# Performance work log

Hardware: AMD Instinct MI355X
Metric: run time of the kernel (lower is better)

The kernel has to match this reference:

```python
import jax, jax.numpy as jnp
import numpy as np


def setup_inputs() -> dict:
    key = jax.random.key(0)
    k1, k2, k3, k4 = jax.random.split(key, 4)
    B, T, N, C_IN, C_OUT, K = 32, 24, 1024, 64, 64, 3
    x = jax.random.normal(k1, (B, T, N, C_IN), dtype=jnp.float32)
    Tks = jax.random.normal(k2, (K, N, N), dtype=jnp.float32)
    # kaiming-uniform-ish init scale for Theta, small uniform bias
    bound_t = float(np.sqrt(6.0 / C_IN))
    Theta = jax.random.uniform(k3, (K, C_IN, C_OUT), dtype=jnp.float32,
                               minval=-bound_t, maxval=bound_t)
    bound_b = 1.0 / float(np.sqrt(C_IN))
    bias = jax.random.uniform(k4, (K, C_OUT), dtype=jnp.float32,
                              minval=-bound_b, maxval=bound_b)
    return {"x": x, "Tks": Tks, "Theta": Theta, "bias": bias}


def reference(x, Tks, Theta, bias):
    # torch.einsum('nn,btnc->btnc', T_k, x) extracts diag(T_k) and scales x per node.
    d = jnp.diagonal(Tks, axis1=1, axis2=2)  # [K, N]
    # sum_k diag(T_k) * x @ Theta_k  -> [B, T, N, C_OUT]
    out = jnp.einsum('kn,btnc,kco->btno', d, x, Theta)
    # each bias[k] is added once -> total additive term is sum over k
    out = out + jnp.sum(bias, axis=0)
    return out
```

## Files before the change

### kernel.cpp

```cpp
#include <hip/hip_runtime.h>


#define NNODES 1024
#define TILE_ROWS 64
#define NT 8
#define ROWS_PER_BLOCK (TILE_ROWS * NT)
#define NBLOCKS (786432 / ROWS_PER_BLOCK)

#define WS_W  0
#define WS_BS (24 * 1024)
#define WS_DV (24 * 1024 + 256)

typedef __attribute__((ext_vector_type(8))) short short8;
typedef __attribute__((ext_vector_type(4))) float f32x4;
typedef __attribute__((ext_vector_type(4))) int   i32x4;

__device__ __forceinline__ unsigned short f2bf(float f) {
    union { float f; unsigned u; } v; v.f = f;
    unsigned r = v.u + 0x7FFFu + ((v.u >> 16) & 1u);
    return (unsigned short)(r >> 16);
}

__device__ __forceinline__ int cvt_pk_bf16(float lo, float hi) {
    int r;
    asm("v_cvt_pk_bf16_f32 %0, %1, %2" : "=v"(r) : "v"(lo), "v"(hi));
    return r;
}

__device__ __forceinline__ void gload_lds16(const void* g, void* l) {
    __builtin_amdgcn_global_load_lds(
        (const __attribute__((address_space(1))) void*)g,
        (__attribute__((address_space(3))) void*)l,
        16, 0, 0);
}

__global__ void cheb_prep(const float* __restrict__ Tks,
                          const float* __restrict__ Theta,
                          const float* __restrict__ bias,
                          unsigned char* __restrict__ ws) {
    const int b = blockIdx.x;
    const int l = threadIdx.x;
    if (b < 24) {
        const int kc = b >> 3, h = (b >> 2) & 1, nb = b & 3;
        const int o  = nb * 16 + (l & 15);
        const int cb = h * 32 + (l >> 4) * 8;
        unsigned short* dst = (unsigned short*)(ws + WS_W) + ((size_t)b * 64 + l) * 8;
        #pragma unroll
        for (int j = 0; j < 8; ++j)
            dst[j] = f2bf(Theta[kc * 4096 + (cb + j) * 64 + o]);
    } else if (b < 40) {
        const int n = (b - 24) * 64 + l;
        const size_t dg = (size_t)n * (NNODES + 1);
        f32x4 v;
        v[0] = Tks[dg];
        v[1] = Tks[(size_t)NNODES * NNODES + dg];
        v[2] = Tks[(size_t)2 * NNODES * NNODES + dg];
        v[3] = 0.0f;
        *((f32x4*)(ws + WS_DV) + n) = v;
    } else {
        float* bs = (float*)(ws + WS_BS);
        bs[l] = bias[l] + bias[64 + l] + bias[128 + l];
    }
}

__global__ __launch_bounds__(512, 4) void cheb_main(
    const float* __restrict__ x,
    const unsigned char* __restrict__ ws,
    float* __restrict__ out)
{
    __shared__ float xs[4][TILE_ROWS * 64];
    __shared__ __align__(16) float dvs[ROWS_PER_BLOCK][4];

    const int tid  = threadIdx.x;
    const int wave = tid >> 6;
    const int lane = tid & 63;
    const int lrow = lane & 15;
    const int lgrp = lane >> 4;
    const int wr   = wave >> 1;
    const int q    = wave & 1;
    const size_t rowbase = (size_t)blockIdx.x * ROWS_PER_BLOCK;

    const unsigned short* wimg = (const unsigned short*)(ws + WS_W);
    const float*          bsum = (const float*)(ws + WS_BS);
    const f32x4*          dvec = (const f32x4*)(ws + WS_DV);

    short8 wf[3][2][2];
    #pragma unroll
    for (int kc = 0; kc < 3; ++kc)
        #pragma unroll
        for (int h = 0; h < 2; ++h)
            #pragma unroll
            for (int nb = 0; nb < 2; ++nb)
                wf[kc][h][nb] = *(const short8*)(
                    wimg + ((size_t)(((kc * 2 + h) * 4 + q * 2 + nb) * 64 + lane)) * 8);

    f32x4 bs4[2];
    #pragma unroll
    for (int nb = 0; nb < 2; ++nb)
        bs4[nb] = *(const f32x4*)(bsum + q * 32 + nb * 16 + lgrp * 4);

    gload_lds16((const char*)dvec + (((rowbase + wave * 64) & (NNODES - 1)) * 16 + lane * 16),
                &dvs[wave * 64][0]);

#define STAGE(T) do { if ((T) < NT) {                                         \
        _Pragma("unroll")                                                     \
        for (int s = 0; s < 2; ++s) {                                         \
            const int u_ = wave * 2 + s;                                      \
            const int R_ = u_ * 4 + lgrp;                                     \
            const int c_ = (lrow * 16) ^ ((R_ & 7) << 4);                     \
            const char* g_ = (const char*)x +                                 \
                (((rowbase + (size_t)(T) * TILE_ROWS + R_) << 8) + c_);       \
            gload_lds16(g_, (char*)&xs[(T) & 3][0] + u_ * 1024);              \
        } } } while (0)

#define WAITV(N) do {                                                         \
        asm volatile("s_waitcnt vmcnt(" #N ")" ::: "memory");                 \
        __builtin_amdgcn_sched_barrier(0);                                    \
        __builtin_amdgcn_s_barrier();                                         \
        __builtin_amdgcn_sched_barrier(0);                                    \
    } while (0)

#define BODY(T) do {                                                          \
        const int m_ = (lrow & 7) << 4;                                       \
        const char* rowp = (const char*)&xs[(T) & 3][0]                       \
                         + (wr * 16 + lrow) * 256;                            \
        const int c00 = (lgrp * 32) ^ m_;                                     \
        const int c01 = (lgrp * 32 + 16) ^ m_;                                \
        const f32x4 x0 = *(const f32x4*)(rowp + c00);                         \
        const f32x4 x1 = *(const f32x4*)(rowp + c01);                         \
        const f32x4 x2 = *(const f32x4*)(rowp + 128 + c00);                   \
        const f32x4 x3 = *(const f32x4*)(rowp + 128 + c01);                   \
        const f32x4 dv = *(const f32x4*)(&dvs[(T) * TILE_ROWS                 \
                                              + wr * 16 + lrow][0]);          \
        short8 xf[3][2];                                                      \
        _Pragma("unroll")                                                     \
        for (int kc = 0; kc < 3; ++kc) {                                      \
            const float dk = dv[kc];                                          \
            i32x4 r0, r1;                                                     \
            r0[0] = cvt_pk_bf16(dk * x0[0], dk * x0[1]);                      \
            r0[1] = cvt_pk_bf16(dk * x0[2], dk * x0[3]);                      \
            r0[2] = cvt_pk_bf16(dk * x1[0], dk * x1[1]);                      \
            r0[3] = cvt_pk_bf16(dk * x1[2], dk * x1[3]);                      \
            r1[0] = cvt_pk_bf16(dk * x2[0], dk * x2[1]);                      \
            r1[1] = cvt_pk_bf16(dk * x2[2], dk * x2[3]);                      \
            r1[2] = cvt_pk_bf16(dk * x3[0], dk * x3[1]);                      \
            r1[3] = cvt_pk_bf16(dk * x3[2], dk * x3[3]);                      \
            xf[kc][0] = __builtin_bit_cast(short8, r0);                       \
            xf[kc][1] = __builtin_bit_cast(short8, r1);                       \
        }                                                                     \
        f32x4 acc[2] = {f32x4{0,0,0,0}, f32x4{0,0,0,0}};                      \
        __builtin_amdgcn_s_setprio(1);                                        \
        _Pragma("unroll")                                                     \
        for (int kc = 0; kc < 3; ++kc)                                        \
            _Pragma("unroll")                                                 \
            for (int h = 0; h < 2; ++h)                                       \
                _Pragma("unroll")                                             \
                for (int nb = 0; nb < 2; ++nb)                                \
                    acc[nb] = __builtin_amdgcn_mfma_f32_16x16x32_bf16(        \
                        wf[kc][h][nb], xf[kc][h], acc[nb], 0, 0, 0);          \
        __builtin_amdgcn_s_setprio(0);                                        \
        float* orow = out + (rowbase + (size_t)(T) * TILE_ROWS                \
                           + wr * 16 + lrow) * 64 + q * 32;                   \
        _Pragma("unroll")                                                     \
        for (int nb = 0; nb < 2; ++nb) {                                      \
            f32x4 o4;                                                         \
            _Pragma("unroll")                                                 \
            for (int j = 0; j < 4; ++j) o4[j] = acc[nb][j] + bs4[nb][j];      \
            __builtin_nontemporal_store(o4, (f32x4*)(orow + nb * 16 + lgrp * 4)); \
        }                                                                     \
    } while (0)

    STAGE(0); STAGE(1); STAGE(2);
    WAITV(2); STAGE(3);  BODY(0);
    WAITV(4); STAGE(4);  BODY(1);
    WAITV(6); STAGE(5);  BODY(2);
    WAITV(6); STAGE(6);  BODY(3);
    WAITV(6); STAGE(7);  BODY(4);
    WAITV(6); STAGE(8);  BODY(5);
    WAITV(6); STAGE(9);  BODY(6);
    WAITV(4); STAGE(10); BODY(7);

#undef STAGE
#undef WAITV
#undef BODY
}

extern "C" void kernel_launch(void* const* d_in, const int* in_sizes, int n_in,
                              void* d_out, int out_size, void* d_ws, size_t ws_size,
                              hipStream_t stream) {
    const float* x     = (const float*)d_in[0];
    const float* Tks   = (const float*)d_in[1];
    const float* Theta = (const float*)d_in[2];
    const float* bias  = (const float*)d_in[3];
    float* out = (float*)d_out;
    unsigned char* ws = (unsigned char*)d_ws;

    hipLaunchKernelGGL(cheb_prep, dim3(41), dim3(64), 0, stream,
                       Tks, Theta, bias, ws);
    hipLaunchKernelGGL(cheb_main, dim3(NBLOCKS), dim3(512), 0, stream,
                       x, ws, out);
}
```

Before: 85.44 us.

## Stage outputs through LDS for coalesced row stores with software-pipelined epilogue

Each wave now writes its MFMA accumulators plus bias into the swizzled LDS x-tile slot it has just consumed. In the next pipeline step the tile is read back row-wise and stored to global memory as full contiguous 256-byte rows, replacing the strided per-lane nontemporal stores. Accumulators alternate between two register sets so the write-out of tile T overlaps the compute of tile T+1. Prefetch depth drops from three tiles in flight to two, and the waits now also drain LDS operations, which adds barrier and LDS traffic.

```diff
diff --git a/kernel.cpp b/kernel.cpp
--- a/kernel.cpp
+++ b/kernel.cpp
@@ -114,13 +114,20 @@
         } } } while (0)
 
 #define WAITV(N) do {                                                         \
-        asm volatile("s_waitcnt vmcnt(" #N ")" ::: "memory");                 \
+        asm volatile("s_waitcnt vmcnt(" #N ") lgkmcnt(0)" ::: "memory");      \
         __builtin_amdgcn_sched_barrier(0);                                    \
         __builtin_amdgcn_s_barrier();                                         \
         __builtin_amdgcn_sched_barrier(0);                                    \
     } while (0)
 
-#define BODY(T) do {                                                          \
+#define WAITL() do {                                                          \
+        asm volatile("s_waitcnt lgkmcnt(0)" ::: "memory");                    \
+        __builtin_amdgcn_sched_barrier(0);                                    \
+        __builtin_amdgcn_s_barrier();                                         \
+        __builtin_amdgcn_sched_barrier(0);                                    \
+    } while (0)
+
+#define BODY(T, A0, A1) do {                                                  \
         const int m_ = (lrow & 7) << 4;                                       \
         const char* rowp = (const char*)&xs[(T) & 3][0]                       \
                          + (wr * 16 + lrow) * 256;                            \
@@ -148,41 +155,61 @@
             xf[kc][0] = __builtin_bit_cast(short8, r0);                       \
             xf[kc][1] = __builtin_bit_cast(short8, r1);                       \
         }                                                                     \
-        f32x4 acc[2] = {f32x4{0,0,0,0}, f32x4{0,0,0,0}};                      \
+        A0 = f32x4{0,0,0,0}; A1 = f32x4{0,0,0,0};                             \
         __builtin_amdgcn_s_setprio(1);                                        \
         _Pragma("unroll")                                                     \
         for (int kc = 0; kc < 3; ++kc)                                        \
             _Pragma("unroll")                                                 \
-            for (int h = 0; h < 2; ++h)                                       \
-                _Pragma("unroll")                                             \
-                for (int nb = 0; nb < 2; ++nb)                                \
-                    acc[nb] = __builtin_amdgcn_mfma_f32_16x16x32_bf16(        \
-                        wf[kc][h][nb], xf[kc][h], acc[nb], 0, 0, 0);          \
+            for (int h = 0; h < 2; ++h) {                                     \
+                A0 = __builtin_amdgcn_mfma_f32_16x16x32_bf16(                 \
+                         wf[kc][h][0], xf[kc][h], A0, 0, 0, 0);               \
+                A1 = __builtin_amdgcn_mfma_f32_16x16x32_bf16(                 \
+                         wf[kc][h][1], xf[kc][h], A1, 0, 0, 0);               \
+            }                                                                 \
         __builtin_amdgcn_s_setprio(0);                                        \
-        float* orow = out + (rowbase + (size_t)(T) * TILE_ROWS                \
-                           + wr * 16 + lrow) * 64 + q * 32;                   \
-        _Pragma("unroll")                                                     \
-        for (int nb = 0; nb < 2; ++nb) {                                      \
-            f32x4 o4;                                                         \
-            _Pragma("unroll")                                                 \
-            for (int j = 0; j < 4; ++j) o4[j] = acc[nb][j] + bs4[nb][j];      \
-            __builtin_nontemporal_store(o4, (f32x4*)(orow + nb * 16 + lgrp * 4)); \
-        }                                                                     \
-    } while (0)
-
-    STAGE(0); STAGE(1); STAGE(2);
-    WAITV(2); STAGE(3);  BODY(0);
-    WAITV(4); STAGE(4);  BODY(1);
-    WAITV(6); STAGE(5);  BODY(2);
-    WAITV(6); STAGE(6);  BODY(3);
-    WAITV(6); STAGE(7);  BODY(4);
-    WAITV(6); STAGE(8);  BODY(5);
-    WAITV(6); STAGE(9);  BODY(6);
-    WAITV(4); STAGE(10); BODY(7);
+    } while (0)
+
+#define WOUT(T, A0, A1) do {                                                  \
+        char* pb = (char*)&xs[(T) & 3][0] + wr * 4096 + lrow * 256;           \
+        const int sw = (lrow & 7) << 4;                                       \
+        f32x4 o0, o1;                                                         \
+        _Pragma("unroll")                                                     \
+        for (int j = 0; j < 4; ++j) { o0[j] = A0[j] + bs4[0][j];              \
+                                      o1[j] = A1[j] + bs4[1][j]; }            \
+        *(f32x4*)(pb + ((q * 128 + 0  + lgrp * 16) ^ sw)) = o0;               \
+        *(f32x4*)(pb + ((q * 128 + 64 + lgrp * 16) ^ sw)) = o1;               \
+    } while (0)
+
+#define EPILOG(T) do {                                                        \
+        _Pragma("unroll")                                                     \
+        for (int s = 0; s < 2; ++s) {                                         \
+            const int row = q * 8 + s * 4 + lgrp;                             \
+            const f32x4 v = *(const f32x4*)((const char*)&xs[(T) & 3][0]      \
+                + wr * 4096 + row * 256 + ((lrow * 16) ^ ((row & 7) << 4)));  \
+            *(f32x4*)(out + (rowbase + (size_t)(T) * TILE_ROWS + wr * 16      \
+                             + row) * 64 + lrow * 4) = v;                     \
+        } } while (0)
+
+    f32x4 accA0, accA1, accB0, accB1;
+
+    STAGE(0); STAGE(1);
+    WAITV(2);            STAGE(2);            BODY(0, accA0, accA1);
+    WAITV(2);            STAGE(3); WOUT(0, accA0, accA1); BODY(1, accB0, accB1);
+    WAITV(2); EPILOG(0); STAGE(4); WOUT(1, accB0, accB1); BODY(2, accA0, accA1);
+    WAITV(4); EPILOG(1); STAGE(5); WOUT(2, accA0, accA1); BODY(3, accB0, accB1);
+    WAITV(4); EPILOG(2); STAGE(6); WOUT(3, accB0, accB1); BODY(4, accA0, accA1);
+    WAITV(4); EPILOG(3); STAGE(7); WOUT(4, accA0, accA1); BODY(5, accB0, accB1);
+    WAITV(4); EPILOG(4);           WOUT(5, accB0, accB1); BODY(6, accA0, accA1);
+    WAITV(2); EPILOG(5);           WOUT(6, accA0, accA1); BODY(7, accB0, accB1);
+    WAITL();  EPILOG(6);           WOUT(7, accB0, accB1);
+    WAITL();  EPILOG(7);
 
 #undef STAGE
 #undef WAITV
+#undef WAITL
 #undef BODY
+#undef WOUT
+#undef EPILOG
 }
 
 extern "C" void kernel_launch(void* const* d_in, const int* in_sizes, int n_in,
```

New measurement: 87.89 us. 2.9% more time.
